# Kernel tuning notes

Measured on AMD Instinct MI355X. Metric: run time of the kernel, lower is better.

## Reference

```python
import jax, jax.numpy as jnp
import numpy as np

K = 5            # local_window_size
S = K * K + 1    # num_affinity_samples = 26


def _local_indices(H, W, k):
    # Mirrors generate_local_indices: reflection-pad an arange index map and
    # unfold kxk windows -> [H*W, k*k] flat node indices.
    p = (k - 1) // 2
    idx = np.arange(H * W, dtype=np.int64).reshape(H, W)
    idx = np.pad(idx, p, mode='reflect')
    win = np.lib.stride_tricks.sliding_window_view(idx, (k, k))  # [H,W,k,k]
    return win.reshape(H * W, k * k)


def setup_inputs() -> dict:
    key = jax.random.key(0)
    ks = jax.random.split(key, 8)
    B, C, H, W = 4, 64, 128, 128
    D = 64  # kq_dim
    s = 1.0 / np.sqrt(C)
    return {
        'x': jax.random.normal(ks[0], (B, C, H, W), jnp.float32),
        'conv_w': jax.random.normal(ks[1], (D, C), jnp.float32) * s,
        'conv_b': jax.random.normal(ks[2], (D,), jnp.float32) * 0.01,
        'key_w': jax.random.normal(ks[3], (D, D), jnp.float32) * s,
        'key_b': jax.random.normal(ks[4], (D,), jnp.float32) * 0.01,
        'query_w': jax.random.normal(ks[5], (D, D), jnp.float32) * s,
        'query_b': jax.random.normal(ks[6], (D,), jnp.float32) * 0.01,
        'rand_global_inds': jax.random.randint(ks[7], (B, H * W, S - K * K), 0, H * W).astype(jnp.int64),
    }


def reference(x, conv_w, conv_b, key_w, key_b, query_w, query_b, rand_global_inds):
    B, C, H, W = x.shape
    HW = H * W
    # 1x1 conv (kq_conv): [B,C,H,W] -> [B,H,W,D]
    kq = jnp.einsum('bchw,dc->bhwd', x, conv_w) + conv_b
    # keys/query decoders (torch Linear: y = x W^T + b), flattened to [B,HW,D]
    keys = (kq @ key_w.T + key_b).reshape(B, HW, -1)
    queries = (kq @ query_w.T + query_b).reshape(B, HW, -1)
    # sample indices: 25 local window neighbors + 1 random global per node
    local = jnp.asarray(_local_indices(H, W, K))                 # [HW, 25]
    local = jnp.broadcast_to(local[None], (B, HW, K * K))
    sample_inds = jnp.concatenate([local, rand_global_inds], -1)  # [B,HW,S]
    # gather keys at sampled indices: [B,HW,S,D]
    gathered_key = jax.vmap(lambda k, idx: k[idx])(keys, sample_inds)
    # per-sample dot product with the node's own query, scaled by C^-0.5
    logits = jnp.einsum('bnd,bnsd->bns', queries, gathered_key) * (C ** -0.5)
    return logits
```

## Files before the change

### kernel.cpp

```cpp
#include <hip/hip_runtime.h>
#include <hip/hip_bf16.h>

#define HW 16384
#define NB 4

typedef __attribute__((ext_vector_type(8))) short bf16x8;
typedef __attribute__((ext_vector_type(4))) float f32x4;

__device__ __forceinline__ float blo(unsigned u) { return __uint_as_float(u << 16); }
__device__ __forceinline__ float bhi(unsigned u) { return __uint_as_float(u & 0xffff0000u); }


__global__ __launch_bounds__(256) void combine_weights(
    const float* __restrict__ conv_w, const float* __restrict__ conv_b,
    const float* __restrict__ key_w, const float* __restrict__ key_b,
    const float* __restrict__ query_w, const float* __restrict__ query_b,
    ushort* __restrict__ Wb, float* __restrict__ bout) {
    __shared__ float cw[4096];
    __shared__ float wr[4][64];
    __shared__ float cb[64];
    int t = threadIdx.x, bx = blockIdx.x;
    int sel = bx >> 4, d0 = (bx & 15) * 4;
    const float* Wm = sel ? query_w : key_w;
    for (int i = t; i < 4096; i += 256) cw[i] = conv_w[i];
    wr[t >> 6][t & 63] = Wm[d0 * 64 + t];
    if (t < 64) cb[t] = conv_b[t];
    __syncthreads();
    int dd = t >> 6, c = t & 63;
    float acc = 0.f;
    #pragma unroll 8
    for (int k = 0; k < 64; ++k) acc += wr[dd][k] * cw[k * 64 + c];
    __hip_bfloat16 h = __float2bfloat16(acc);
    Wb[(sel * 64 + d0 + dd) * 64 + c] = *(ushort*)&h;
    if (t < 4) {
        float bacc = 0.f;
        for (int k = 0; k < 64; ++k) bacc += wr[t][k] * cb[k];
        bacc += (sel ? query_b : key_b)[d0 + t];
        bout[sel * 64 + d0 + t] = bacc;
    }
}

__global__ __launch_bounds__(256, 2) void gemm_kq(
    const float* __restrict__ x, const ushort* __restrict__ W,
    const float* __restrict__ bias, ushort* __restrict__ keys,
    ushort* __restrict__ queries) {
    __shared__ ushort xs[256 * 64];
    __shared__ ushort epi[256 * 64];
    __shared__ float bs[128];
    int t = threadIdx.x;
    int b = blockIdx.x >> 6;
    int n0 = (blockIdx.x & 63) << 8;

    if (t < 128) bs[t] = bias[t];
    {
        const float* xp = x + ((size_t)b << 20) + n0 + t;
        unsigned u[32];
        #pragma unroll
        for (int cc = 0; cc < 32; ++cc) {
            float lo = xp[(size_t)(2 * cc) * HW];
            float hi = xp[(size_t)(2 * cc + 1) * HW];
            __hip_bfloat162 h2 = __float22bfloat162_rn(make_float2(lo, hi));
            u[cc] = *(unsigned*)&h2;
        }
        #pragma unroll
        for (int q = 0; q < 8; ++q)
            *(uint4*)((char*)xs + t * 128 + (((q ^ (t & 7))) << 4)) =
                make_uint4(u[4 * q], u[4 * q + 1], u[4 * q + 2], u[4 * q + 3]);
    }
    __syncthreads();

    int l = t & 63, w = t >> 6;
    int ncol = l & 15, kg = l >> 4;

    bf16x8 Bf[4][2];
    #pragma unroll
    for (int nt = 0; nt < 4; ++nt) {
        int row = w * 64 + nt * 16 + ncol;
        #pragma unroll
        for (int half = 0; half < 2; ++half) {
            int q = half * 4 + kg;
            Bf[nt][half] = *(bf16x8*)((char*)xs + row * 128 + ((q ^ (row & 7)) << 4));
        }
    }

    f32x4 acc[8][4];
    #pragma unroll
    for (int dt = 0; dt < 8; ++dt)
        #pragma unroll
        for (int nt = 0; nt < 4; ++nt) acc[dt][nt] = (f32x4){0.f, 0.f, 0.f, 0.f};

    #pragma unroll
    for (int dt = 0; dt < 8; ++dt) {
        const bf16x8* arow = (const bf16x8*)(W + (dt * 16 + ncol) * 64 + kg * 8);
        bf16x8 A0 = arow[0];
        bf16x8 A1 = arow[4];
        #pragma unroll
        for (int nt = 0; nt < 4; ++nt) {
            acc[dt][nt] = __builtin_amdgcn_mfma_f32_16x16x32_bf16(A0, Bf[nt][0], acc[dt][nt], 0, 0, 0);
            acc[dt][nt] = __builtin_amdgcn_mfma_f32_16x16x32_bf16(A1, Bf[nt][1], acc[dt][nt], 0, 0, 0);
        }
    }

    #pragma unroll
    for (int p = 0; p < 2; ++p) {
        #pragma unroll
        for (int dt = 0; dt < 4; ++dt) {
            int dbase = dt * 16 + kg * 4;
            float4 bb = *(float4*)&bs[p * 64 + dbase];
            #pragma unroll
            for (int nt = 0; nt < 4; ++nt) {
                int n = w * 64 + nt * 16 + ncol;
                f32x4 a = acc[p * 4 + dt][nt];
                __hip_bfloat162 lo2 = __float22bfloat162_rn(make_float2(a[0] + bb.x, a[1] + bb.y));
                __hip_bfloat162 hi2 = __float22bfloat162_rn(make_float2(a[2] + bb.z, a[3] + bb.w));
                *(uint2*)((char*)epi + n * 128 + (((dbase >> 3) ^ (n & 7)) << 4) + ((dbase & 4) << 1)) =
                    make_uint2(*(unsigned*)&lo2, *(unsigned*)&hi2);
            }
        }
        __syncthreads();
        ushort* dst = p ? queries : keys;
        #pragma unroll
        for (int i = 0; i < 8; ++i) {
            int idx = i * 256 + t;
            int row = idx >> 3, ch = idx & 7;
            uint4 v = *(uint4*)((char*)epi + row * 128 + ((ch ^ (row & 7)) << 4));
            *(uint4*)(dst + (((size_t)(b * HW + n0 + row)) << 6) + ch * 8) = v;
        }
        __syncthreads();
    }
}

__global__ __launch_bounds__(256) void affinity(
    const ushort* __restrict__ keys, const ushort* __restrict__ queries,
    const int* __restrict__ rnd, float* __restrict__ out) {
    __shared__ float res[416];
    int t = threadIdx.x;
    int b = blockIdx.x >> 10;
    int n0 = (blockIdx.x & 1023) << 4;

    int j = t & 3;
    int g = t >> 2;
    int n_loc = g & 15;
    int sb = g >> 4;
    int n = n0 + n_loc;

    const uint4* qp = (const uint4*)(queries + (((size_t)(b * HW + n)) << 6) + j * 16);
    uint4 qa = qp[0], qb = qp[1];
    float qf[16];
    qf[0] = blo(qa.x); qf[1] = bhi(qa.x); qf[2] = blo(qa.y); qf[3] = bhi(qa.y);
    qf[4] = blo(qa.z); qf[5] = bhi(qa.z); qf[6] = blo(qa.w); qf[7] = bhi(qa.w);
    qf[8] = blo(qb.x); qf[9] = bhi(qb.x); qf[10] = blo(qb.y); qf[11] = bhi(qb.y);
    qf[12] = blo(qb.z); qf[13] = bhi(qb.z); qf[14] = blo(qb.w); qf[15] = bhi(qb.w);

    int y = n >> 7, xq = n & 127;
    const ushort* kb_ = keys + (((size_t)b * HW) << 6) + j * 16;
    int rix = rnd[b * HW + n];

    #pragma unroll
    for (int k = 0; k < 7; ++k) {
        int s = sb + 4 * k;
        if (s < 26) {
            int idxn;
            if (s < 25) {
                int q5 = s / 5;
                int dy = q5 - 2, dx = s - q5 * 5 - 2;
                int ry = y + dy;
                ry = ry < 0 ? -ry : (ry > 127 ? 254 - ry : ry);
                int rx = xq + dx;
                rx = rx < 0 ? -rx : (rx > 127 ? 254 - rx : rx);
                idxn = (ry << 7) + rx;
            } else {
                idxn = rix;
            }
            const uint4* kp = (const uint4*)(kb_ + ((size_t)idxn << 6));
            uint4 ka = kp[0], kc = kp[1];
            float a = 0.f;
            a = fmaf(blo(ka.x), qf[0], a);  a = fmaf(bhi(ka.x), qf[1], a);
            a = fmaf(blo(ka.y), qf[2], a);  a = fmaf(bhi(ka.y), qf[3], a);
            a = fmaf(blo(ka.z), qf[4], a);  a = fmaf(bhi(ka.z), qf[5], a);
            a = fmaf(blo(ka.w), qf[6], a);  a = fmaf(bhi(ka.w), qf[7], a);
            a = fmaf(blo(kc.x), qf[8], a);  a = fmaf(bhi(kc.x), qf[9], a);
            a = fmaf(blo(kc.y), qf[10], a); a = fmaf(bhi(kc.y), qf[11], a);
            a = fmaf(blo(kc.z), qf[12], a); a = fmaf(bhi(kc.z), qf[13], a);
            a = fmaf(blo(kc.w), qf[14], a); a = fmaf(bhi(kc.w), qf[15], a);
            a += __shfl_xor(a, 1);
            a += __shfl_xor(a, 2);
            if (j == 0) res[n_loc * 26 + s] = a * 0.125f;
        }
    }
    __syncthreads();
    size_t ob = ((size_t)(b * HW + n0)) * 26;
    out[ob + t] = res[t];
    if (t < 160) out[ob + 256 + t] = res[256 + t];
}

extern "C" void kernel_launch(void* const* d_in, const int* in_sizes, int n_in,
                              void* d_out, int out_size, void* d_ws, size_t ws_size,
                              hipStream_t stream) {
    const float* x       = (const float*)d_in[0];
    const float* conv_w  = (const float*)d_in[1];
    const float* conv_b  = (const float*)d_in[2];
    const float* key_w   = (const float*)d_in[3];
    const float* key_b   = (const float*)d_in[4];
    const float* query_w = (const float*)d_in[5];
    const float* query_b = (const float*)d_in[6];
    const int*   rnd     = (const int*)d_in[7];
    float* out = (float*)d_out;

    ushort* Wb    = (ushort*)d_ws;
    float*  biasp = (float*)((char*)d_ws + 16384);
    ushort* keys  = (ushort*)((char*)d_ws + 32768);
    ushort* quer  = keys + (size_t)NB * HW * 64;

    combine_weights<<<32, 256, 0, stream>>>(conv_w, conv_b, key_w, key_b,
                                            query_w, query_b, Wb, biasp);
    gemm_kq<<<NB * (HW / 256), 256, 0, stream>>>(x, Wb, biasp, keys, quer);
    affinity<<<NB * (HW / 16), 256, 0, stream>>>(keys, quer, rnd, out);
}
```

Baseline: 37.11 us.

## Shrink GEMM tiles, drop LDS staging in weight combine, specialize affinity samples

```diff
diff --git a/kernel.cpp b/kernel.cpp
--- a/kernel.cpp
+++ b/kernel.cpp
@@ -16,89 +16,76 @@
     const float* __restrict__ key_w, const float* __restrict__ key_b,
     const float* __restrict__ query_w, const float* __restrict__ query_b,
     ushort* __restrict__ Wb, float* __restrict__ bout) {
-    __shared__ float cw[4096];
-    __shared__ float wr[4][64];
-    __shared__ float cb[64];
     int t = threadIdx.x, bx = blockIdx.x;
     int sel = bx >> 4, d0 = (bx & 15) * 4;
     const float* Wm = sel ? query_w : key_w;
-    for (int i = t; i < 4096; i += 256) cw[i] = conv_w[i];
-    wr[t >> 6][t & 63] = Wm[d0 * 64 + t];
-    if (t < 64) cb[t] = conv_b[t];
-    __syncthreads();
     int dd = t >> 6, c = t & 63;
+    const float* wrow = Wm + (d0 + dd) * 64;
     float acc = 0.f;
-    #pragma unroll 8
-    for (int k = 0; k < 64; ++k) acc += wr[dd][k] * cw[k * 64 + c];
+    #pragma unroll
+    for (int k = 0; k < 64; ++k) acc = fmaf(wrow[k], conv_w[k * 64 + c], acc);
     __hip_bfloat16 h = __float2bfloat16(acc);
     Wb[(sel * 64 + d0 + dd) * 64 + c] = *(ushort*)&h;
     if (t < 4) {
+        const float* wr2 = Wm + (d0 + t) * 64;
         float bacc = 0.f;
-        for (int k = 0; k < 64; ++k) bacc += wr[t][k] * cb[k];
+        #pragma unroll
+        for (int k = 0; k < 64; ++k) bacc = fmaf(wr2[k], conv_b[k], bacc);
         bacc += (sel ? query_b : key_b)[d0 + t];
         bout[sel * 64 + d0 + t] = bacc;
     }
 }
 
-__global__ __launch_bounds__(256, 2) void gemm_kq(
+__global__ __launch_bounds__(256) void gemm_kq(
     const float* __restrict__ x, const ushort* __restrict__ W,
     const float* __restrict__ bias, ushort* __restrict__ keys,
     ushort* __restrict__ queries) {
-    __shared__ ushort xs[256 * 64];
-    __shared__ ushort epi[256 * 64];
+    __shared__ ushort xs[64 * 64];
+    __shared__ ushort epi[64 * 64];
     __shared__ float bs[128];
     int t = threadIdx.x;
-    int b = blockIdx.x >> 6;
-    int n0 = (blockIdx.x & 63) << 8;
+    int b = blockIdx.x >> 8;
+    int n0 = (blockIdx.x & 255) << 6;
 
     if (t < 128) bs[t] = bias[t];
     {
-        const float* xp = x + ((size_t)b << 20) + n0 + t;
-        unsigned u[32];
-        #pragma unroll
-        for (int cc = 0; cc < 32; ++cc) {
+        int r = t & 63, q0 = t >> 6;
+        const float* xp = x + ((size_t)(b * 64 + q0 * 16)) * HW + n0 + r;
+        unsigned u[8];
+        #pragma unroll
+        for (int cc = 0; cc < 8; ++cc) {
             float lo = xp[(size_t)(2 * cc) * HW];
             float hi = xp[(size_t)(2 * cc + 1) * HW];
             __hip_bfloat162 h2 = __float22bfloat162_rn(make_float2(lo, hi));
             u[cc] = *(unsigned*)&h2;
         }
         #pragma unroll
-        for (int q = 0; q < 8; ++q)
-            *(uint4*)((char*)xs + t * 128 + (((q ^ (t & 7))) << 4)) =
+        for (int q = 0; q < 2; ++q) {
+            int qq = q0 * 2 + q;
+            *(uint4*)((char*)xs + r * 128 + ((qq ^ (r & 7)) << 4)) =
                 make_uint4(u[4 * q], u[4 * q + 1], u[4 * q + 2], u[4 * q + 3]);
+        }
     }
     __syncthreads();
 
     int l = t & 63, w = t >> 6;
     int ncol = l & 15, kg = l >> 4;
 
-    bf16x8 Bf[4][2];
-    #pragma unroll
-    for (int nt = 0; nt < 4; ++nt) {
-        int row = w * 64 + nt * 16 + ncol;
-        #pragma unroll
-        for (int half = 0; half < 2; ++half) {
-            int q = half * 4 + kg;
-            Bf[nt][half] = *(bf16x8*)((char*)xs + row * 128 + ((q ^ (row & 7)) << 4));
-        }
-    }
-
-    f32x4 acc[8][4];
-    #pragma unroll
-    for (int dt = 0; dt < 8; ++dt)
-        #pragma unroll
-        for (int nt = 0; nt < 4; ++nt) acc[dt][nt] = (f32x4){0.f, 0.f, 0.f, 0.f};
+    bf16x8 Bf[2];
+    int brow = w * 16 + ncol;
+    #pragma unroll
+    for (int half = 0; half < 2; ++half)
+        Bf[half] = *(bf16x8*)((char*)xs + brow * 128 + (((half * 4 + kg) ^ (brow & 7)) << 4));
+
+    f32x4 acc[8];
+    #pragma unroll
+    for (int dt = 0; dt < 8; ++dt) acc[dt] = (f32x4){0.f, 0.f, 0.f, 0.f};
 
     #pragma unroll
     for (int dt = 0; dt < 8; ++dt) {
         const bf16x8* arow = (const bf16x8*)(W + (dt * 16 + ncol) * 64 + kg * 8);
-        bf16x8 A0 = arow[0];
-        bf16x8 A1 = arow[4];
-        #pragma unroll
-        for (int nt = 0; nt < 4; ++nt) {
-            acc[dt][nt] = __builtin_amdgcn_mfma_f32_16x16x32_bf16(A0, Bf[nt][0], acc[dt][nt], 0, 0, 0);
-            acc[dt][nt] = __builtin_amdgcn_mfma_f32_16x16x32_bf16(A1, Bf[nt][1], acc[dt][nt], 0, 0, 0);
-        }
+        acc[dt] = __builtin_amdgcn_mfma_f32_16x16x32_bf16(arow[0], Bf[0], acc[dt], 0, 0, 0);
+        acc[dt] = __builtin_amdgcn_mfma_f32_16x16x32_bf16(arow[4], Bf[1], acc[dt], 0, 0, 0);
     }
 
     #pragma unroll
@@ -107,20 +94,17 @@
         for (int dt = 0; dt < 4; ++dt) {
             int dbase = dt * 16 + kg * 4;
             float4 bb = *(float4*)&bs[p * 64 + dbase];
-            #pragma unroll
-            for (int nt = 0; nt < 4; ++nt) {
-                int n = w * 64 + nt * 16 + ncol;
-                f32x4 a = acc[p * 4 + dt][nt];
-                __hip_bfloat162 lo2 = __float22bfloat162_rn(make_float2(a[0] + bb.x, a[1] + bb.y));
-                __hip_bfloat162 hi2 = __float22bfloat162_rn(make_float2(a[2] + bb.z, a[3] + bb.w));
-                *(uint2*)((char*)epi + n * 128 + (((dbase >> 3) ^ (n & 7)) << 4) + ((dbase & 4) << 1)) =
-                    make_uint2(*(unsigned*)&lo2, *(unsigned*)&hi2);
-            }
+            int n = w * 16 + ncol;
+            f32x4 a = acc[p * 4 + dt];
+            __hip_bfloat162 lo2 = __float22bfloat162_rn(make_float2(a[0] + bb.x, a[1] + bb.y));
+            __hip_bfloat162 hi2 = __float22bfloat162_rn(make_float2(a[2] + bb.z, a[3] + bb.w));
+            *(uint2*)((char*)epi + n * 128 + (((dbase >> 3) ^ (n & 7)) << 4) + ((dbase & 4) << 1)) =
+                make_uint2(*(unsigned*)&lo2, *(unsigned*)&hi2);
         }
         __syncthreads();
         ushort* dst = p ? queries : keys;
         #pragma unroll
-        for (int i = 0; i < 8; ++i) {
+        for (int i = 0; i < 2; ++i) {
             int idx = i * 256 + t;
             int row = idx >> 3, ch = idx & 7;
             uint4 v = *(uint4*)((char*)epi + row * 128 + ((ch ^ (row & 7)) << 4));
@@ -129,6 +113,33 @@
         __syncthreads();
     }
 }
+
+#define DOT(s_, idxn_) do {                                                   \
+    const uint4* kp = (const uint4*)(kb_ + ((size_t)(idxn_) << 6));           \
+    uint4 ka = kp[0], kc = kp[1];                                             \
+    float a = 0.f;                                                            \
+    a = fmaf(blo(ka.x), qf[0], a);  a = fmaf(bhi(ka.x), qf[1], a);            \
+    a = fmaf(blo(ka.y), qf[2], a);  a = fmaf(bhi(ka.y), qf[3], a);            \
+    a = fmaf(blo(ka.z), qf[4], a);  a = fmaf(bhi(ka.z), qf[5], a);            \
+    a = fmaf(blo(ka.w), qf[6], a);  a = fmaf(bhi(ka.w), qf[7], a);            \
+    a = fmaf(blo(kc.x), qf[8], a);  a = fmaf(bhi(kc.x), qf[9], a);            \
+    a = fmaf(blo(kc.y), qf[10], a); a = fmaf(bhi(kc.y), qf[11], a);           \
+    a = fmaf(blo(kc.z), qf[12], a); a = fmaf(bhi(kc.z), qf[13], a);           \
+    a = fmaf(blo(kc.w), qf[14], a); a = fmaf(bhi(kc.w), qf[15], a);           \
+    a += __shfl_xor(a, 1);                                                    \
+    a += __shfl_xor(a, 2);                                                    \
+    if (j == 0) res[n_loc * 26 + (s_)] = a * 0.125f;                          \
+} while (0)
+
+#define SAMP(s_, dy_, dx_) do {                                               \
+    int ry = y + (dy_);                                                       \
+    if ((dy_) < 0) ry = (ry < 0) ? -ry : ry;                                  \
+    if ((dy_) > 0) ry = (ry > 127) ? 254 - ry : ry;                           \
+    int rx = xq + (dx_);                                                      \
+    if ((dx_) < 0) rx = (rx < 0) ? -rx : rx;                                  \
+    if ((dx_) > 0) rx = (rx > 127) ? 254 - rx : rx;                           \
+    DOT(s_, (ry << 7) + rx);                                                  \
+} while (0)
 
 __global__ __launch_bounds__(256) void affinity(
     const ushort* __restrict__ keys, const ushort* __restrict__ queries,
@@ -154,39 +165,27 @@
 
     int y = n >> 7, xq = n & 127;
     const ushort* kb_ = keys + (((size_t)b * HW) << 6) + j * 16;
-    int rix = rnd[b * HW + n];
-
-    #pragma unroll
-    for (int k = 0; k < 7; ++k) {
-        int s = sb + 4 * k;
-        if (s < 26) {
-            int idxn;
-            if (s < 25) {
-                int q5 = s / 5;
-                int dy = q5 - 2, dx = s - q5 * 5 - 2;
-                int ry = y + dy;
-                ry = ry < 0 ? -ry : (ry > 127 ? 254 - ry : ry);
-                int rx = xq + dx;
-                rx = rx < 0 ? -rx : (rx > 127 ? 254 - rx : rx);
-                idxn = (ry << 7) + rx;
-            } else {
-                idxn = rix;
-            }
-            const uint4* kp = (const uint4*)(kb_ + ((size_t)idxn << 6));
-            uint4 ka = kp[0], kc = kp[1];
-            float a = 0.f;
-            a = fmaf(blo(ka.x), qf[0], a);  a = fmaf(bhi(ka.x), qf[1], a);
-            a = fmaf(blo(ka.y), qf[2], a);  a = fmaf(bhi(ka.y), qf[3], a);
-            a = fmaf(blo(ka.z), qf[4], a);  a = fmaf(bhi(ka.z), qf[5], a);
-            a = fmaf(blo(ka.w), qf[6], a);  a = fmaf(bhi(ka.w), qf[7], a);
-            a = fmaf(blo(kc.x), qf[8], a);  a = fmaf(bhi(kc.x), qf[9], a);
-            a = fmaf(blo(kc.y), qf[10], a); a = fmaf(bhi(kc.y), qf[11], a);
-            a = fmaf(blo(kc.z), qf[12], a); a = fmaf(bhi(kc.z), qf[13], a);
-            a = fmaf(blo(kc.w), qf[14], a); a = fmaf(bhi(kc.w), qf[15], a);
-            a += __shfl_xor(a, 1);
-            a += __shfl_xor(a, 2);
-            if (j == 0) res[n_loc * 26 + s] = a * 0.125f;
-        }
+
+    switch (sb) {
+    case 0:
+        SAMP(0, -2, -2); SAMP(4, -2, 2);  SAMP(8, -1, 1);  SAMP(12, 0, 0);
+        SAMP(16, 1, -1); SAMP(20, 2, -2); SAMP(24, 2, 2);
+        break;
+    case 1: {
+        SAMP(1, -2, -1); SAMP(5, -1, -2); SAMP(9, -1, 2);  SAMP(13, 0, 1);
+        SAMP(17, 1, 0);  SAMP(21, 2, -1);
+        int rix = rnd[b * HW + n];
+        DOT(25, rix);
+        break;
+    }
+    case 2:
+        SAMP(2, -2, 0);  SAMP(6, -1, -1); SAMP(10, 0, -2); SAMP(14, 0, 2);
+        SAMP(18, 1, 1);  SAMP(22, 2, 0);
+        break;
+    default:
+        SAMP(3, -2, 1);  SAMP(7, -1, 0);  SAMP(11, 0, -1); SAMP(15, 1, -2);
+        SAMP(19, 1, 2);  SAMP(23, 2, 1);
+        break;
     }
     __syncthreads();
     size_t ob = ((size_t)(b * HW + n0)) * 26;
@@ -214,6 +213,6 @@
 
     combine_weights<<<32, 256, 0, stream>>>(conv_w, conv_b, key_w, key_b,
                                             query_w, query_b, Wb, biasp);
-    gemm_kq<<<NB * (HW / 256), 256, 0, stream>>>(x, Wb, biasp, keys, quer);
+    gemm_kq<<<NB * (HW / 64), 256, 0, stream>>>(x, Wb, biasp, keys, quer);
     affinity<<<NB * (HW / 16), 256, 0, stream>>>(keys, quer, rnd, out);
 }
```

Result: slower. 38.71 us (+4.3%).
